# Kernel optimization log

Measured on AMD Instinct MI355X. Metric: run time of the kernel, lower is better.

The kernel has to match this reference:

```python
import jax, jax.numpy as jnp
import numpy as np

NUM_HEADS = 16
HEAD_CH = 64
D_MODEL = 1024  # == NUM_HEADS*HEAD_CH -> out_mapper is Identity


def setup_inputs() -> dict:
    key = jax.random.key(0)
    k1, k2, k3 = jax.random.split(key, 3)
    tokens = jax.random.normal(k1, (2, 2048, D_MODEL), dtype=jnp.float32)
    w_qkv = jax.random.normal(k2, (D_MODEL, 3 * D_MODEL), dtype=jnp.float32) * (1.0 / np.sqrt(D_MODEL))
    b_qkv = jax.random.normal(k3, (3 * D_MODEL,), dtype=jnp.float32) * 0.02
    return {"tokens": tokens, "w_qkv": w_qkv, "b_qkv": b_qkv}


def reference(tokens, w_qkv, b_qkv):
    b, n, _ = tokens.shape
    qkv = tokens @ w_qkv + b_qkv  # [b, n, 3*inner]
    q, k, v = jnp.split(qkv, 3, axis=-1)

    def heads(x):  # [b, n, h*d] -> [b, h, n, d]
        return x.reshape(b, n, NUM_HEADS, HEAD_CH).transpose(0, 2, 1, 3)

    q, k, v = heads(q), heads(k), heads(v)
    scores = jnp.einsum('bhqd,bhkd->bhqk', q, k) / jnp.sqrt(jnp.float32(HEAD_CH))
    attn = jax.nn.softmax(scores, axis=-1)
    out = jnp.einsum('bhqk,bhkd->bhqd', attn, v)  # [b, h, n, d]
    out = out.transpose(0, 2, 1, 3).reshape(b, n, NUM_HEADS * HEAD_CH)
    return out  # out_mapper is Identity since inner_channels == input_channels
```

## Files before the change

kernel.cpp:

```cpp
#include <hip/hip_runtime.h>
#include <stdint.h>

typedef __attribute__((ext_vector_type(8))) short shortx8;
typedef __attribute__((ext_vector_type(4))) float floatx4;
typedef unsigned short bf16_t;

#define NH 16
#define HD 64
#define SEQ 2048
#define BATCH 2
#define DM 1024
#define DM3 3072

#define GLDS(gp, lp) __builtin_amdgcn_global_load_lds( \
    (const __attribute__((address_space(1))) unsigned int*)(gp), \
    (__attribute__((address_space(3))) unsigned int*)(lp), 16, 0, 0)

__device__ __forceinline__ bf16_t f2bf(float f) {
    unsigned int u = __float_as_uint(f);
    u += 0x7fff + ((u >> 16) & 1);
    return (bf16_t)(u >> 16);
}
__device__ __forceinline__ unsigned pk2bf(float lo, float hi) {
    return (unsigned)f2bf(lo) | ((unsigned)f2bf(hi) << 16);
}

__global__ __launch_bounds__(256) void conv_all(const float* __restrict__ tokens,
                                                bf16_t* __restrict__ tok_bf,
                                                const float* __restrict__ w,
                                                bf16_t* __restrict__ wt) {
    __shared__ bf16_t t[64 * 65];
    const int bx = blockIdx.x, tid = threadIdx.x;
    if (bx < 2048) {
        int idx = bx * 256 + tid;
        float4 a = ((const float4*)tokens)[idx * 2];
        float4 b = ((const float4*)tokens)[idx * 2 + 1];
        uint4 o;
        o.x = pk2bf(a.x, a.y);
        o.y = pk2bf(a.z, a.w);
        o.z = pk2bf(b.x, b.y);
        o.w = pk2bf(b.z, b.w);
        ((uint4*)tok_bf)[idx] = o;
    } else {
        const int bw = bx - 2048;
        const int n0 = (bw % 48) * 64, k0 = (bw / 48) * 64;
        for (int i = 0; i < 16; i++) {
            int idx = i * 256 + tid;
            int r = idx >> 6, c = idx & 63;
            t[r * 65 + c] = f2bf(w[(k0 + r) * DM3 + n0 + c]);
        }
        __syncthreads();
        for (int i = 0; i < 16; i++) {
            int idx = i * 256 + tid;
            int r = idx >> 6, c = idx & 63;
            wt[(n0 + r) * DM + k0 + c] = t[c * 65 + r];
        }
    }
}


#define QSCALE 0.18033688011f

template<bool SW>
__device__ __forceinline__ void kloop(const bf16_t* __restrict__ A, const bf16_t* __restrict__ Bt,
                                      bf16_t* __restrict__ As, bf16_t* __restrict__ Bs,
                                      int m0, int n0, floatx4 (&acc)[4][4]) {
    const int tid = threadIdx.x;
    const int wave = tid >> 6, lane = tid & 63;
    const int quad = lane >> 4, l16 = lane & 15;
    const int wm = (wave & 1) * 64, wn = (wave >> 1) * 64;
    const int srow = tid >> 3;
    const int swz8 = ((tid & 7) ^ (srow & 7)) * 8;
    const int h3 = l16 & 7;
    for (int kt = 0; kt < DM; kt += 64) {
        __syncthreads();
        for (int rr = 0; rr < 4; rr++) {
            GLDS(&A[(m0 + rr * 32 + srow) * DM + kt + swz8], &As[rr * 2048 + tid * 8]);
            GLDS(&Bt[(n0 + rr * 32 + srow) * DM + kt + swz8], &Bs[rr * 2048 + tid * 8]);
        }
        __syncthreads();
        for (int ks = 0; ks < 2; ks++) {
            const int g = ((ks * 4 + quad) ^ h3) * 8;
            shortx8 af[4], bfr[4];
            for (int t = 0; t < 4; t++)
                af[t] = *(const shortx8*)&As[(wm + t * 16 + l16) * 64 + g];
            for (int t = 0; t < 4; t++)
                bfr[t] = *(const shortx8*)&Bs[(wn + t * 16 + l16) * 64 + g];
            for (int i = 0; i < 4; i++)
                for (int j = 0; j < 4; j++)
                    acc[i][j] = SW
                        ? __builtin_amdgcn_mfma_f32_16x16x32_bf16(bfr[j], af[i], acc[i][j], 0, 0, 0)
                        : __builtin_amdgcn_mfma_f32_16x16x32_bf16(af[i], bfr[j], acc[i][j], 0, 0, 0);
        }
    }
}

__global__ __launch_bounds__(256) void qkv_gemm(const bf16_t* __restrict__ A,
                                                const bf16_t* __restrict__ Bt,
                                                const float* __restrict__ bias,
                                                bf16_t* __restrict__ Qo,
                                                bf16_t* __restrict__ Ko,
                                                bf16_t* __restrict__ Vto) {
    __shared__ __align__(16) char smem[128 * 136 * 2];
    bf16_t* As = (bf16_t*)smem;
    bf16_t* Bs = As + 128 * 64;
    bf16_t* Cs = (bf16_t*)smem;
    const int m0 = blockIdx.x * 128;
    const int n0 = blockIdx.y * 128;
    const int tid = threadIdx.x;
    const int wave = tid >> 6, lane = tid & 63;
    const int quad = lane >> 4, l16 = lane & 15;
    const int wm = (wave & 1) * 64, wn = (wave >> 1) * 64;
    const int part = n0 >> 10;
    const int b = m0 >> 11, pos0 = m0 & 2047;
    floatx4 acc[4][4] = {};

    if (part != 2) {
        kloop<true>(A, Bt, As, Bs, m0, n0, acc);
        __syncthreads();
        for (int i = 0; i < 4; i++) {
            int ml = wm + i * 16 + l16;
            for (int j = 0; j < 4; j++) {
                int nl = wn + j * 16 + quad * 4;
                float4 bv = *(const float4*)&bias[n0 + nl];
                float v0 = acc[i][j][0] + bv.x, v1 = acc[i][j][1] + bv.y;
                float v2 = acc[i][j][2] + bv.z, v3 = acc[i][j][3] + bv.w;
                if (part == 0) { v0 *= QSCALE; v1 *= QSCALE; v2 *= QSCALE; v3 *= QSCALE; }
                uint2 pk;
                pk.x = pk2bf(v0, v1);
                pk.y = pk2bf(v2, v3);
                *(uint2*)&Cs[ml * 136 + nl] = pk;
            }
        }
        __syncthreads();
        bf16_t* dst = (part == 0) ? Qo : Ko;
        for (int p = 0; p < 8; p++) {
            int ml = p * 16 + (tid >> 4);
            int g = tid & 15;
            uint4 v = *(const uint4*)&Cs[ml * 136 + g * 8];
            int rr = (n0 + g * 8) & 1023;
            int h = rr >> 6, d = rr & 63;
            *(uint4*)&dst[(size_t)((b * NH + h) * SEQ + pos0 + ml) * HD + d] = v;
        }
    } else {
        kloop<false>(A, Bt, As, Bs, m0, n0, acc);
        __syncthreads();
        for (int i = 0; i < 4; i++)
            for (int j = 0; j < 4; j++) {
                int nl = wn + j * 16 + l16;
                float bv = bias[n0 + nl];
                uint2 pk;
                pk.x = pk2bf(acc[i][j][0] + bv, acc[i][j][1] + bv);
                pk.y = pk2bf(acc[i][j][2] + bv, acc[i][j][3] + bv);
                *(uint2*)&Cs[nl * 136 + wm + i * 16 + quad * 4] = pk;
            }
        __syncthreads();
        for (int p = 0; p < 8; p++) {
            int nl = p * 16 + (tid >> 4);
            int g = tid & 15;
            uint4 v = *(const uint4*)&Cs[nl * 136 + g * 8];
            int rr = (n0 + nl) & 1023;
            int h = rr >> 6, d = rr & 63;
            *(uint4*)&Vto[(size_t)((b * NH + h) * HD + d) * SEQ + pos0 + g * 8] = v;
        }
    }
}

__global__ __launch_bounds__(256, 2) void attn(const bf16_t* __restrict__ Q,
                                               const bf16_t* __restrict__ K,
                                               const bf16_t* __restrict__ Vt,
                                               float* __restrict__ out) {
    __shared__ __align__(16) char smem[65536];
    bf16_t* Ks = (bf16_t*)smem;
    bf16_t* Vs = (bf16_t*)(smem + 16384);
    bf16_t* Ps = (bf16_t*)(smem + 32768);

    const int bh = blockIdx.x;
    const int qt_blk = blockIdx.y;
    const int b = bh >> 4, h = bh & 15;
    const int q0 = qt_blk * 128;
    const bf16_t* Qb = Q + ((size_t)bh * SEQ + q0) * HD;
    const bf16_t* Kb = K + (size_t)bh * SEQ * HD;
    const bf16_t* Vb = Vt + (size_t)bh * HD * SEQ;
    const int tid = threadIdx.x;
    const int wave = tid >> 6, lane = tid & 63;
    const int quad = lane >> 4, l16 = lane & 15;
    const int h3 = l16 & 7;
    const int qh = wave >> 1, kh = wave & 1;
    bf16_t* Pw = Ps + wave * 4096;

    const int srow = tid >> 3;
    const int sg8 = ((tid & 7) ^ (srow & 7)) * 8;
    const int vrow = tid >> 4;
    const int vg8 = (((tid & 15) ^ vrow) & 15) * 8;

    shortx8 qf[4][2];
    for (int qt = 0; qt < 4; qt++)
        for (int kc = 0; kc < 2; kc++)
            qf[qt][kc] = *(const shortx8*)&Qb[(qh * 64 + qt * 16 + l16) * 64 + kc * 32 + quad * 8];

    shortx8 ones;
    for (int i = 0; i < 8; i++) ones[i] = (short)0x3F80;

    const floatx4 minit = {-12.f, -12.f, -12.f, -12.f};
    floatx4 acc_l[4] = {};
    floatx4 acc_o[4][4] = {};

    for (int rr = 0; rr < 4; rr++) {
        GLDS(&Kb[(rr * 32 + srow) * 64 + sg8], &Ks[rr * 2048 + tid * 8]);
        GLDS(&Vb[(size_t)(rr * 16 + vrow) * SEQ + vg8], &Vs[rr * 2048 + tid * 8]);
    }
    __syncthreads();

    for (int it = 0; it < SEQ / 128; ++it) {
        shortx8 kf[2][4], vf[2][4];
        for (int kc = 0; kc < 2; kc++) {
            const int g = ((kc * 4 + quad) ^ h3) * 8;
            for (int kt = 0; kt < 4; kt++)
                kf[kc][kt] = *(const shortx8*)&Ks[(kh * 64 + kt * 16 + l16) * 64 + g];
        }
        for (int hp = 0; hp < 2; hp++)
            for (int dt = 0; dt < 4; dt++)
                vf[hp][dt] = *(const shortx8*)&Vs[(dt * 16 + l16) * 128 +
                                                  (((kh * 8 + hp * 4 + quad) ^ l16) & 15) * 8];
        __syncthreads();
        if (it + 1 < SEQ / 128) {
            const int kk = (it + 1) * 128;
            for (int rr = 0; rr < 4; rr++) {
                GLDS(&Kb[(kk + rr * 32 + srow) * 64 + sg8], &Ks[rr * 2048 + tid * 8]);
                GLDS(&Vb[(size_t)(rr * 16 + vrow) * SEQ + kk + vg8], &Vs[rr * 2048 + tid * 8]);
            }
        }

        for (int hp = 0; hp < 2; hp++) {
            floatx4 s[2][4];
            for (int k2 = 0; k2 < 2; k2++)
                for (int qt = 0; qt < 4; qt++) s[k2][qt] = minit;
            for (int kc = 0; kc < 2; kc++)
                for (int k2 = 0; k2 < 2; k2++)
                    for (int qt = 0; qt < 4; qt++)
                        s[k2][qt] = __builtin_amdgcn_mfma_f32_16x16x32_bf16(
                            kf[kc][hp * 2 + k2], qf[qt][kc], s[k2][qt], 0, 0, 0);
            for (int qt = 0; qt < 4; qt++)
                for (int k2 = 0; k2 < 2; k2++) {
                    unsigned u[4];
                    for (int r = 0; r < 4; r++)
                        u[r] = __float_as_uint(__builtin_amdgcn_exp2f(s[k2][qt][r])) + 0x8000u;
                    uint2 pk;
                    pk.x = __builtin_amdgcn_perm(u[1], u[0], 0x07060302u);
                    pk.y = __builtin_amdgcn_perm(u[3], u[2], 0x07060302u);
                    *(uint2*)&Pw[(qt * 16 + l16) * 64 +
                                 (((hp * 2 + k2) * 2 + (quad >> 1)) ^ h3) * 8 + (quad & 1) * 4] = pk;
                }
            const int gp = ((hp * 4 + quad) ^ h3) * 8;
            for (int qt = 0; qt < 4; qt++) {
                shortx8 pf = *(const shortx8*)&Pw[(qt * 16 + l16) * 64 + gp];
                acc_l[qt] = __builtin_amdgcn_mfma_f32_16x16x32_bf16(ones, pf, acc_l[qt], 0, 0, 0);
                for (int dt = 0; dt < 4; dt++)
                    acc_o[dt][qt] = __builtin_amdgcn_mfma_f32_16x16x32_bf16(vf[hp][dt], pf, acc_o[dt][qt], 0, 0, 0);
            }
        }
        __syncthreads();
    }

    float* Osh = (float*)smem;
    float* ml = (float*)(smem + 32768);
    if (kh == 1) {
        for (int qt = 0; qt < 4; qt++) {
            for (int dt = 0; dt < 4; dt++) {
                float4 o;
                o.x = acc_o[dt][qt][0]; o.y = acc_o[dt][qt][1];
                o.z = acc_o[dt][qt][2]; o.w = acc_o[dt][qt][3];
                *(float4*)&Osh[qh * 4096 + (qt * 16 + l16) * 64 +
                               (((dt * 4 + quad) ^ l16) & 15) * 4] = o;
            }
            if (quad == 0) ml[(qh * 4 + qt) * 16 + l16] = acc_l[qt][0];
        }
    }
    __syncthreads();
    if (kh == 0) {
        for (int qt = 0; qt < 4; qt++) {
            float l1 = ml[(qh * 4 + qt) * 16 + l16];
            float inv = 1.0f / (acc_l[qt][0] + l1);
            int q = q0 + qh * 64 + qt * 16 + l16;
            for (int dt = 0; dt < 4; dt++) {
                float4 o1 = *(const float4*)&Osh[qh * 4096 + (qt * 16 + l16) * 64 +
                                                 (((dt * 4 + quad) ^ l16) & 15) * 4];
                float4 o;
                o.x = (acc_o[dt][qt][0] + o1.x) * inv;
                o.y = (acc_o[dt][qt][1] + o1.y) * inv;
                o.z = (acc_o[dt][qt][2] + o1.z) * inv;
                o.w = (acc_o[dt][qt][3] + o1.w) * inv;
                *(float4*)&out[(size_t)(b * SEQ + q) * DM + h * HD + dt * 16 + quad * 4] = o;
            }
        }
    }
}

extern "C" void kernel_launch(void* const* d_in, const int* in_sizes, int n_in,
                              void* d_out, int out_size, void* d_ws, size_t ws_size,
                              hipStream_t stream) {
    const float* tokens = (const float*)d_in[0];
    const float* w = (const float*)d_in[1];
    const float* bias = (const float*)d_in[2];
    float* out = (float*)d_out;
    char* ws = (char*)d_ws;

    bf16_t* tok_bf = (bf16_t*)(ws);
    bf16_t* wt_bf  = (bf16_t*)(ws + (size_t)8 * 1024 * 1024);
    bf16_t* Qb     = (bf16_t*)(ws + (size_t)14 * 1024 * 1024);
    bf16_t* Kb     = (bf16_t*)(ws + (size_t)22 * 1024 * 1024);
    bf16_t* Vb     = (bf16_t*)(ws + (size_t)30 * 1024 * 1024);

    conv_all<<<2816, 256, 0, stream>>>(tokens, tok_bf, w, wt_bf);
    qkv_gemm<<<dim3(32, 24), 256, 0, stream>>>(tok_bf, wt_bf, bias, Qb, Kb, Vb);
    attn<<<dim3(32, 16), 256, 0, stream>>>(Qb, Kb, Vb, out);
}
```

Measured before the change: 162.5 us.

## Double-buffer LDS tiles in QKV GEMM k-loop to overlap loads with MFMA

The QKV projection k-loop now uses two LDS buffers for the A and B tiles. The global-to-LDS loads for the next k-step are issued before the MFMAs run on the current one, with one barrier per iteration instead of two. This is meant to hide global memory latency behind matrix math in the GEMM. In exchange, shared memory per block grows to 64KB, which may lower blocks per CU, and the attention kernels are untouched.

```diff
diff --git a/kernel.cpp b/kernel.cpp
--- a/kernel.cpp
+++ b/kernel.cpp
@@ -63,7 +63,7 @@
 
 template<bool SW>
 __device__ __forceinline__ void kloop(const bf16_t* __restrict__ A, const bf16_t* __restrict__ Bt,
-                                      bf16_t* __restrict__ As, bf16_t* __restrict__ Bs,
+                                      bf16_t* __restrict__ smem,
                                       int m0, int n0, floatx4 (&acc)[4][4]) {
     const int tid = threadIdx.x;
     const int wave = tid >> 6, lane = tid & 63;
@@ -72,20 +72,30 @@
     const int srow = tid >> 3;
     const int swz8 = ((tid & 7) ^ (srow & 7)) * 8;
     const int h3 = l16 & 7;
-    for (int kt = 0; kt < DM; kt += 64) {
-        __syncthreads();
-        for (int rr = 0; rr < 4; rr++) {
-            GLDS(&A[(m0 + rr * 32 + srow) * DM + kt + swz8], &As[rr * 2048 + tid * 8]);
-            GLDS(&Bt[(n0 + rr * 32 + srow) * DM + kt + swz8], &Bs[rr * 2048 + tid * 8]);
-        }
-        __syncthreads();
+    bf16_t* As[2] = { smem, smem + 8192 };
+    bf16_t* Bs[2] = { smem + 16384, smem + 24576 };
+
+    for (int rr = 0; rr < 4; rr++) {
+        GLDS(&A[(m0 + rr * 32 + srow) * DM + swz8], &As[0][rr * 2048 + tid * 8]);
+        GLDS(&Bt[(n0 + rr * 32 + srow) * DM + swz8], &Bs[0][rr * 2048 + tid * 8]);
+    }
+    for (int it = 0; it < 16; it++) {
+        const int cur = it & 1;
+        __syncthreads();
+        if (it + 1 < 16) {
+            const int kt = (it + 1) * 64, nxt = cur ^ 1;
+            for (int rr = 0; rr < 4; rr++) {
+                GLDS(&A[(m0 + rr * 32 + srow) * DM + kt + swz8], &As[nxt][rr * 2048 + tid * 8]);
+                GLDS(&Bt[(n0 + rr * 32 + srow) * DM + kt + swz8], &Bs[nxt][rr * 2048 + tid * 8]);
+            }
+        }
         for (int ks = 0; ks < 2; ks++) {
             const int g = ((ks * 4 + quad) ^ h3) * 8;
             shortx8 af[4], bfr[4];
             for (int t = 0; t < 4; t++)
-                af[t] = *(const shortx8*)&As[(wm + t * 16 + l16) * 64 + g];
+                af[t] = *(const shortx8*)&As[cur][(wm + t * 16 + l16) * 64 + g];
             for (int t = 0; t < 4; t++)
-                bfr[t] = *(const shortx8*)&Bs[(wn + t * 16 + l16) * 64 + g];
+                bfr[t] = *(const shortx8*)&Bs[cur][(wn + t * 16 + l16) * 64 + g];
             for (int i = 0; i < 4; i++)
                 for (int j = 0; j < 4; j++)
                     acc[i][j] = SW
@@ -93,6 +103,7 @@
                         : __builtin_amdgcn_mfma_f32_16x16x32_bf16(af[i], bfr[j], acc[i][j], 0, 0, 0);
         }
     }
+    __syncthreads();
 }
 
 __global__ __launch_bounds__(256) void qkv_gemm(const bf16_t* __restrict__ A,
@@ -101,10 +112,8 @@
                                                 bf16_t* __restrict__ Qo,
                                                 bf16_t* __restrict__ Ko,
                                                 bf16_t* __restrict__ Vto) {
-    __shared__ __align__(16) char smem[128 * 136 * 2];
-    bf16_t* As = (bf16_t*)smem;
-    bf16_t* Bs = As + 128 * 64;
-    bf16_t* Cs = (bf16_t*)smem;
+    __shared__ __align__(16) bf16_t smem[32768];
+    bf16_t* Cs = smem;
     const int m0 = blockIdx.x * 128;
     const int n0 = blockIdx.y * 128;
     const int tid = threadIdx.x;
@@ -116,8 +125,7 @@
     floatx4 acc[4][4] = {};
 
     if (part != 2) {
-        kloop<true>(A, Bt, As, Bs, m0, n0, acc);
-        __syncthreads();
+        kloop<true>(A, Bt, smem, m0, n0, acc);
         for (int i = 0; i < 4; i++) {
             int ml = wm + i * 16 + l16;
             for (int j = 0; j < 4; j++) {
@@ -143,8 +151,7 @@
             *(uint4*)&dst[(size_t)((b * NH + h) * SEQ + pos0 + ml) * HD + d] = v;
         }
     } else {
-        kloop<false>(A, Bt, As, Bs, m0, n0, acc);
-        __syncthreads();
+        kloop<false>(A, Bt, smem, m0, n0, acc);
         for (int i = 0; i < 4; i++)
             for (int j = 0; j < 4; j++) {
                 int nl = wn + j * 16 + l16;
```

Measured after the change: 165.6 us. Within noise of the previous version (+2.0%).
